# Kernel optimization log

Hardware: AMD Instinct MI355X
Metric: run time of the kernel (lower is better)

## Reference

```python
import jax, jax.numpy as jnp
import numpy as np

DIM = 3072
HEADS = 24
HD = 128  # head_dim
RANK = 64
COND = 1024      # (512//8)*(512//8)*16//64
BLOCK = 2048     # main latent tokens
SEQ = BLOCK + COND
NIP = 64         # image_emb tokens
LORA_W = 1.0     # lora_weights[0]
ALPHA_SCALE = 1.0  # network_alpha / rank = 64/64
IP_SCALE = 1.0


def setup_inputs() -> dict:
    key = jax.random.key(0)
    ks = jax.random.split(key, 21)
    d = {}
    d["hidden_states"] = jax.random.normal(ks[0], (1, SEQ, DIM), jnp.float32)
    d["image_emb"] = jax.random.normal(ks[1], (1, NIP, DIM), jnp.float32)
    d["rope_cos"] = jax.random.uniform(ks[2], (SEQ, HD), jnp.float32)
    d["rope_sin"] = jax.random.uniform(ks[3], (SEQ, HD), jnp.float32)
    d["wq"] = jax.random.normal(ks[4], (DIM, DIM), jnp.float32) * 0.02
    d["bq"] = jax.random.normal(ks[5], (DIM,), jnp.float32) * 0.02
    d["wk"] = jax.random.normal(ks[6], (DIM, DIM), jnp.float32) * 0.02
    d["bk"] = jax.random.normal(ks[7], (DIM,), jnp.float32) * 0.02
    d["wv"] = jax.random.normal(ks[8], (DIM, DIM), jnp.float32) * 0.02
    d["bv"] = jax.random.normal(ks[9], (DIM,), jnp.float32) * 0.02
    d["norm_q_w"] = jax.random.uniform(ks[10], (HD,), jnp.float32, 0.5, 1.5)
    d["norm_k_w"] = jax.random.uniform(ks[11], (HD,), jnp.float32, 0.5, 1.5)
    d["q_down"] = jax.random.normal(ks[12], (RANK, DIM), jnp.float32) / RANK
    d["q_up"] = jax.random.normal(ks[13], (DIM, RANK), jnp.float32) * 0.02
    d["k_down"] = jax.random.normal(ks[14], (RANK, DIM), jnp.float32) / RANK
    d["k_up"] = jax.random.normal(ks[15], (DIM, RANK), jnp.float32) * 0.02
    d["v_down"] = jax.random.normal(ks[16], (RANK, DIM), jnp.float32) / RANK
    d["v_up"] = jax.random.normal(ks[17], (DIM, RANK), jnp.float32) * 0.02
    d["wk_ip"] = jax.random.normal(ks[18], (DIM, DIM), jnp.float32) * 0.02
    d["wv_ip"] = jax.random.normal(ks[19], (DIM, DIM), jnp.float32) * 0.02
    return d


def _rmsnorm(x, w, eps):
    v = jnp.mean(jnp.square(x), axis=-1, keepdims=True)
    y = x * jax.lax.rsqrt(v + eps)
    return y if w is None else y * w


def _heads(x, b):  # (B,S,DIM) -> (B,H,S,HD)
    return x.reshape(b, -1, HEADS, HD).transpose(0, 2, 1, 3)


def _rope(x, cos, sin):
    # diffusers apply_rotary_emb, use_real, unbind_dim=-1
    x1 = x[..., 0::2]
    x2 = x[..., 1::2]
    rot = jnp.stack([-x2, x1], axis=-1).reshape(x.shape)
    return x * cos[None, None] + rot * sin[None, None]


def _sdpa(q, k, v, bias=None):
    s = jnp.einsum("bhqd,bhkd->bhqk", q, k) / jnp.sqrt(jnp.float32(q.shape[-1]))
    if bias is not None:
        s = s + bias
    p = jax.nn.softmax(s, axis=-1)
    return jnp.einsum("bhqk,bhkd->bhqd", p, v)


def reference(hidden_states, image_emb, rope_cos, rope_sin,
              wq, bq, wk, bk, wv, bv, norm_q_w, norm_k_w,
              q_down, q_up, k_down, k_up, v_down, v_up, wk_ip, wv_ip):
    B = hidden_states.shape[0]

    # base QKV projections
    q = hidden_states @ wq.T + bq
    k = hidden_states @ wk.T + bk
    v = hidden_states @ wv.T + bv

    # original (pre-LoRA, pre-norm, pre-RoPE) query on the main block for IP attention
    original_query = _heads(hidden_states[:, :BLOCK] @ wq.T + bq, B)

    # masked LoRA add (n_loras=1): only tokens [BLOCK, BLOCK+COND) contribute
    pos = jnp.arange(SEQ)
    tok_mask = ((pos >= BLOCK) & (pos < BLOCK + COND)).astype(hidden_states.dtype)
    hm = hidden_states * tok_mask[None, :, None]
    q = q + LORA_W * ALPHA_SCALE * ((hm @ q_down.T) @ q_up.T)
    k = k + LORA_W * ALPHA_SCALE * ((hm @ k_down.T) @ k_up.T)
    v = v + LORA_W * ALPHA_SCALE * ((hm @ v_down.T) @ v_up.T)

    q = _heads(q, B)
    k = _heads(k, B)
    v = _heads(v, B)

    # per-head RMSNorm (attn.norm_q / attn.norm_k, eps=1e-6 in Flux)
    q = _rmsnorm(q, norm_q_w, 1e-6)
    k = _rmsnorm(k, norm_k_w, 1e-6)

    # IP-adapter cross attention with the original query
    ip_k = _rmsnorm(_heads(image_emb @ wk_ip.T, B), None, 1e-5)
    ip_v = _heads(image_emb @ wv_ip.T, B)
    ip_out = _sdpa(original_query, ip_k, ip_v)  # (B,H,BLOCK,HD)
    ip_out = ip_out.transpose(0, 2, 1, 3).reshape(B, -1, DIM)

    # RoPE on q/k
    q = _rope(q, rope_cos, rope_sin)
    k = _rope(k, rope_cos, rope_sin)

    # attention bias: main-block queries see everything; cond queries only their own block
    m = jnp.ones((SEQ, SEQ), jnp.float32)
    m = m.at[:BLOCK, :].set(0.0)
    m = m.at[BLOCK:BLOCK + COND, BLOCK:BLOCK + COND].set(0.0)
    bias = (m * -1e20)[None, None]

    out = _sdpa(q, k, v, bias)  # (B,H,SEQ,HD)
    out = out.transpose(0, 2, 1, 3).reshape(B, SEQ, DIM)

    main = out[:, :BLOCK, :] + IP_SCALE * ip_out
    return main
```

## Files before the change

### kernel.cpp

```cpp
#include <hip/hip_runtime.h>
#include <stdint.h>

#define DIM 3072
#define HEADS 24
#define HD 128
#define RANKN 64
#define CONDN 1024
#define BLK 2048
#define SEQN 3072
#define NIPN 64

typedef __attribute__((ext_vector_type(8))) short s8v;
typedef __attribute__((ext_vector_type(4))) float fx4;

static __device__ __forceinline__ unsigned short f2bf(float f){
  union{float f; unsigned u;} v; v.f=f;
  unsigned r = v.u + 0x7FFFu + ((v.u>>16)&1u);
  return (unsigned short)(r>>16);
}
static __device__ __forceinline__ float bf2f(unsigned short b){
  union{unsigned u; float f;} v; v.u = ((unsigned)b) << 16;
  return v.f;
}

#define GL16(g,l) __builtin_amdgcn_global_load_lds((const __attribute__((address_space(1))) void*)(g), (__attribute__((address_space(3))) void*)(l), 16, 0, 0)
#define MFMA(a,b,c) __builtin_amdgcn_mfma_f32_16x16x32_bf16((a),(b),(c),0,0,0)

__global__ __launch_bounds__(256) void cvt_f32_bf16(const float* __restrict__ src,
                                                    unsigned short* __restrict__ dst, int n4){
  int i = blockIdx.x*256 + threadIdx.x;
  if (i < n4){
    float4 v = ((const float4*)src)[i];
    ushort4 o;
    o.x = f2bf(v.x); o.y = f2bf(v.y); o.z = f2bf(v.z); o.w = f2bf(v.w);
    ((ushort4*)dst)[i] = o;
  }
}

__global__ __launch_bounds__(256) void lora_down_g(const unsigned short* __restrict__ A,
                                                   const unsigned short* __restrict__ D0,
                                                   const unsigned short* __restrict__ D1,
                                                   unsigned short* __restrict__ outb){
  __shared__ unsigned short As[128*64];
  __shared__ unsigned short Bs[64*64];
  int tid = threadIdx.x, lane = tid & 63, w = tid >> 6;
  int l15 = lane & 15, l16 = lane >> 4;
  int z = blockIdx.z;
  int m0 = blockIdx.y * 128;
  const unsigned short* Dw = z ? D1 : D0;
  int wr = w * 32;
  fx4 acc[2][4] = {};
  for (int kt = 0; kt < DIM; kt += 64){
    #pragma unroll
    for (int i = 0; i < 4; i++){
      int p = i*256 + tid;
      int row = p >> 3, cc = p & 7;
      int gc = cc ^ (row & 7);
      GL16(A + (size_t)(m0+row)*DIM + kt + gc*8, As + p*8);
    }
    #pragma unroll
    for (int i = 0; i < 2; i++){
      int p = i*256 + tid;
      int row = p >> 3, cc = p & 7;
      int gc = cc ^ (row & 7);
      GL16(Dw + (size_t)row*DIM + kt + gc*8, Bs + p*8);
    }
    __syncthreads();
    #pragma unroll
    for (int kk = 0; kk < 2; kk++){
      s8v af[2], bfr[4];
      #pragma unroll
      for (int t = 0; t < 2; t++){
        int rowa = wr + t*16 + l15;
        int ca = (kk*4 + l16) ^ (rowa & 7);
        af[t] = *(const s8v*)(As + rowa*64 + ca*8);
      }
      #pragma unroll
      for (int t = 0; t < 4; t++){
        int rowb = t*16 + l15;
        int cb = (kk*4 + l16) ^ (rowb & 7);
        bfr[t] = *(const s8v*)(Bs + rowb*64 + cb*8);
      }
      #pragma unroll
      for (int mt = 0; mt < 2; mt++)
        #pragma unroll
        for (int nt = 0; nt < 4; nt++)
          acc[mt][nt] = MFMA(af[mt], bfr[nt], acc[mt][nt]);
    }
    __syncthreads();
  }
  #pragma unroll
  for (int mt = 0; mt < 2; mt++)
    #pragma unroll
    for (int j = 0; j < 4; j++){
      int row = m0 + wr + mt*16 + l16*4 + j;
      #pragma unroll
      for (int nt = 0; nt < 4; nt++){
        int col = nt*16 + l15;
        outb[((size_t)z*CONDN + row)*64 + col] = f2bf(acc[mt][nt][j]);
      }
    }
}

__global__ __launch_bounds__(512, 2) void gemm_256(
    const unsigned short* __restrict__ hs_bf,
    const unsigned short* __restrict__ ie_bf,
    const unsigned short* __restrict__ Wq,
    const unsigned short* __restrict__ Wk,
    const unsigned short* __restrict__ Wv,
    const unsigned short* __restrict__ Wik,
    const unsigned short* __restrict__ Wiv,
    const float* __restrict__ bq, const float* __restrict__ bk, const float* __restrict__ bv,
    const unsigned short* __restrict__ downb,
    const unsigned short* __restrict__ upk,
    const unsigned short* __restrict__ upv,
    unsigned short* __restrict__ qb, unsigned short* __restrict__ kb, unsigned short* __restrict__ vb,
    float* __restrict__ ipk_pre, float* __restrict__ ipv_pre)
{
  __shared__ unsigned short Ab[2][16384];
  __shared__ unsigned short Bb[2][16384];
  int tid = threadIdx.x, lane = tid & 63, w = tid >> 6;
  int wm = w >> 2, wn = w & 3;
  int l15 = lane & 15, l16 = lane >> 4;

  int b = blockIdx.x;
  int id = (b & 7) * 51 + (b >> 3);
  int z, mt, ntile;
  if (id < 96){ z = 0; mt = id / 12; ntile = id % 12; }
  else if (id < 240){ z = 1; int r = id - 96; mt = r / 12; ntile = r % 12; }
  else if (id < 384){ z = 2; int r = id - 240; mt = r / 12; ntile = r % 12; }
  else { z = 3; int r = id - 384; mt = r / 12; ntile = r % 12; }
  const bool is_ip = (z == 3);
  int z2 = is_ip ? mt : 0;
  int m0 = is_ip ? 0 : mt * 256;
  int n0 = ntile * 256;
  const unsigned short* A = is_ip ? ie_bf : hs_bf;
  const unsigned short* B = is_ip ? (z2 ? Wiv : Wik)
                                  : (z == 0 ? Wq : (z == 1 ? Wk : Wv));

  fx4 acc[8][4] = {};
  s8v af[8], bfr[8];

  auto stA = [&](int buf, int half, int kt){
    #pragma unroll
    for (int i = 0; i < 2; i++){
      int p = i*512 + tid;
      int row = p >> 3, cc = p & 7, gc = cc ^ (row & 7);
      int ar = m0 + half*128 + row;
      if (is_ip && ar > 63) ar = 63;
      GL16(A + (size_t)ar*DIM + kt + gc*8, &Ab[buf][half*8192 + p*8]);
    }
  };
  auto stB = [&](int buf, int half, int kt){
    #pragma unroll
    for (int i = 0; i < 2; i++){
      int p = i*512 + tid;
      int row = p >> 3, cc = p & 7, gc = cc ^ (row & 7);
      GL16(B + (size_t)(n0 + half*128 + row)*DIM + kt + gc*8, &Bb[buf][half*8192 + p*8]);
    }
  };
  auto rdA = [&](int buf, int m, int kk)->s8v{
    int rl = m*16 + l15;
    return *(const s8v*)(&Ab[buf][wm*8192 + rl*64 + ((kk*4 + l16) ^ (rl & 7))*8]);
  };
  auto rdB = [&](int buf, int n, int kk)->s8v{
    int rB = wn*64 + n*16 + l15;
    return *(const s8v*)(&Bb[buf][(rB >> 7)*8192 + (rB & 127)*64 + ((kk*4 + l16) ^ (rB & 7))*8]);
  };

  stA(0,0,0); stA(0,1,0); stB(0,0,0); stB(0,1,0);

  const int NT = DIM / 64;
  for (int t = 0; t < NT; t++){
    int cur = t & 1, nxt = cur ^ 1;
    bool pf = (t + 1 < NT);
    if (pf){
      int kt1 = (t + 1) * 64;
      stA(nxt, 0, kt1); stA(nxt, 1, kt1);
      stB(nxt, 0, kt1); stB(nxt, 1, kt1);
      asm volatile("s_waitcnt vmcnt(8)" ::: "memory");
    } else {
      asm volatile("s_waitcnt vmcnt(0)" ::: "memory");
    }
    __builtin_amdgcn_s_barrier();

    #pragma unroll
    for (int m = 0; m < 4; m++){ af[m*2] = rdA(cur,m,0); af[m*2+1] = rdA(cur,m,1); }
    #pragma unroll
    for (int n = 0; n < 2; n++){ bfr[n*2] = rdB(cur,n,0); bfr[n*2+1] = rdB(cur,n,1); }
    __builtin_amdgcn_s_setprio(1);
    #pragma unroll
    for (int m = 0; m < 4; m++)
      #pragma unroll
      for (int n = 0; n < 2; n++){
        acc[m][n] = MFMA(af[m*2],   bfr[n*2],   acc[m][n]);
        acc[m][n] = MFMA(af[m*2+1], bfr[n*2+1], acc[m][n]);
      }
    __builtin_amdgcn_s_setprio(0);
    #pragma unroll
    for (int n = 2; n < 4; n++){ bfr[n*2] = rdB(cur,n,0); bfr[n*2+1] = rdB(cur,n,1); }
    __builtin_amdgcn_s_setprio(1);
    #pragma unroll
    for (int m = 0; m < 4; m++)
      #pragma unroll
      for (int n = 2; n < 4; n++){
        acc[m][n] = MFMA(af[m*2],   bfr[n*2],   acc[m][n]);
        acc[m][n] = MFMA(af[m*2+1], bfr[n*2+1], acc[m][n]);
      }
    __builtin_amdgcn_s_setprio(0);
    #pragma unroll
    for (int m = 4; m < 8; m++){ af[(m-4)*2] = rdA(cur,m,0); af[(m-4)*2+1] = rdA(cur,m,1); }
    __builtin_amdgcn_s_setprio(1);
    #pragma unroll
    for (int m = 4; m < 8; m++)
      #pragma unroll
      for (int n = 2; n < 4; n++){
        acc[m][n] = MFMA(af[(m-4)*2],   bfr[n*2],   acc[m][n]);
        acc[m][n] = MFMA(af[(m-4)*2+1], bfr[n*2+1], acc[m][n]);
      }
    #pragma unroll
    for (int m = 4; m < 8; m++)
      #pragma unroll
      for (int n = 0; n < 2; n++){
        acc[m][n] = MFMA(af[(m-4)*2],   bfr[n*2],   acc[m][n]);
        acc[m][n] = MFMA(af[(m-4)*2+1], bfr[n*2+1], acc[m][n]);
      }
    __builtin_amdgcn_s_setprio(0);
    __builtin_amdgcn_s_barrier();
  }

  if (is_ip){
    float* outp = z2 ? ipv_pre : ipk_pre;
    if (wm == 0){
      #pragma unroll
      for (int m = 0; m < 4; m++)
        #pragma unroll
        for (int j = 0; j < 4; j++){
          int row = m*16 + l16*4 + j;
          #pragma unroll
          for (int n = 0; n < 4; n++)
            outp[(size_t)row*DIM + n0 + wn*64 + n*16 + l15] = acc[m][n][j];
        }
    }
    return;
  }

  if (z >= 1 && m0 >= BLK){
    const unsigned short* dwn = downb + (size_t)(z-1)*CONDN*64 + (size_t)(m0 - BLK)*64;
    const unsigned short* up  = (z == 1) ? upk : upv;
    #pragma unroll
    for (int i = 0; i < 4; i++){
      int p = i*512 + tid;
      int row = p >> 3, cc = p & 7, gc = cc ^ (row & 7);
      GL16(dwn + (size_t)row*64 + gc*8, &Ab[0][p*8]);
      GL16(up + (size_t)(n0 + row)*64 + gc*8, &Bb[0][p*8]);
    }
    asm volatile("s_waitcnt vmcnt(0)" ::: "memory");
    __builtin_amdgcn_s_barrier();
    #pragma unroll
    for (int kk = 0; kk < 2; kk++){
      s8v aL[8], bL[4];
      #pragma unroll
      for (int m = 0; m < 8; m++){
        int rA = wm*128 + m*16 + l15;
        aL[m] = *(const s8v*)(&Ab[0][rA*64 + ((kk*4 + l16) ^ (rA & 7))*8]);
      }
      #pragma unroll
      for (int n = 0; n < 4; n++){
        int rB = wn*64 + n*16 + l15;
        bL[n] = *(const s8v*)(&Bb[0][rB*64 + ((kk*4 + l16) ^ (rB & 7))*8]);
      }
      #pragma unroll
      for (int m = 0; m < 8; m++)
        #pragma unroll
        for (int n = 0; n < 4; n++)
          acc[m][n] = MFMA(aL[m], bL[n], acc[m][n]);
    }
  }

  {
    const float* bias = z == 0 ? bq : (z == 1 ? bk : bv);
    unsigned short* C = z == 0 ? qb : (z == 1 ? kb : vb);
    float bv4[4];
    #pragma unroll
    for (int n = 0; n < 4; n++) bv4[n] = bias[n0 + wn*64 + n*16 + l15];
    #pragma unroll
    for (int m = 0; m < 8; m++)
      #pragma unroll
      for (int j = 0; j < 4; j++){
        int row = m0 + wm*128 + m*16 + l16*4 + j;
        unsigned short* crow = C + (size_t)row*DIM;
        #pragma unroll
        for (int n = 0; n < 4; n++)
          crow[n0 + wn*64 + n*16 + l15] = f2bf(acc[m][n][j] + bv4[n]);
      }
  }
}

__global__ __launch_bounds__(256) void norm_rope(const unsigned short* __restrict__ src,
                                                 unsigned short* __restrict__ dst,
                                                 const float* __restrict__ wt,
                                                 const float* __restrict__ rc,
                                                 const float* __restrict__ rs,
                                                 int S, float qscale){
  int tid = threadIdx.x, lane = tid & 63, w = tid >> 6;
  int r = blockIdx.x*4 + w;
  int pos = r % S, h = r / S;
  const unsigned short* x = src + (size_t)pos*DIM + h*HD;
  ushort2 xv2 = *(const ushort2*)(x + 2*lane);
  float x0 = bf2f(xv2.x), x1 = bf2f(xv2.y);
  float ss = x0*x0 + x1*x1;
  #pragma unroll
  for (int o = 1; o < 64; o <<= 1) ss += __shfl_xor(ss, o);
  float rr = rsqrtf(ss*(1.f/128.f) + 1e-6f);
  float y0 = x0*rr*wt[2*lane], y1 = x1*rr*wt[2*lane+1];
  float2 cv = *(const float2*)(rc + (size_t)pos*HD + 2*lane);
  float2 sv = *(const float2*)(rs + (size_t)pos*HD + 2*lane);
  float o0 = (y0*cv.x - y1*sv.x)*qscale;
  float o1 = (y1*cv.y + y0*sv.y)*qscale;
  ushort2 ov; ov.x = f2bf(o0); ov.y = f2bf(o1);
  *(ushort2*)(dst + ((size_t)h*S + pos)*HD + 2*lane) = ov;
}

__global__ __launch_bounds__(256) void ipk_norm_bf(const float* __restrict__ src,
                                                   unsigned short* __restrict__ dst){
  int tid = threadIdx.x, lane = tid & 63, w = tid >> 6;
  int r = blockIdx.x*4 + w;
  int pos = r / HEADS, h = r % HEADS;
  const float* x = src + (size_t)pos*DIM + h*HD;
  float2 xv = *(const float2*)(x + 2*lane);
  float ss = xv.x*xv.x + xv.y*xv.y;
  #pragma unroll
  for (int o = 1; o < 64; o <<= 1) ss += __shfl_xor(ss, o);
  float rr = rsqrtf(ss*(1.f/128.f) + 1e-5f);
  ushort2 ov; ov.x = f2bf(xv.x*rr); ov.y = f2bf(xv.y*rr);
  *(ushort2*)(dst + ((size_t)h*NIPN + pos)*HD + 2*lane) = ov;
}

__global__ __launch_bounds__(256) void ipv_transpose(const float* __restrict__ ipv,
                                                     unsigned short* __restrict__ vt){
  int h = blockIdx.x, tid = threadIdx.x;
  #pragma unroll
  for (int i = 0; i < 32; i++){
    int idx = i*256 + tid;
    int d = idx >> 6, key = idx & 63;
    vt[((size_t)h*HD + d)*64 + key] = f2bf(ipv[(size_t)key*DIM + h*HD + d]);
  }
}

__global__ __launch_bounds__(256) void v_transpose(const unsigned short* __restrict__ v,
                                                   unsigned short* __restrict__ Vt){
  __shared__ unsigned short t[64][137];
  int h = blockIdx.y, p0 = blockIdx.x*64, tid = threadIdx.x;
  int dcol = tid & 127, prow2 = tid >> 7;
  #pragma unroll
  for (int i = 0; i < 32; i++){
    int pos = i*2 + prow2;
    t[pos][dcol] = v[(size_t)(p0+pos)*DIM + h*HD + dcol];
  }
  __syncthreads();
  int pos = tid & 63, dbase = tid >> 6;
  #pragma unroll
  for (int i = 0; i < 32; i++){
    int d = i*4 + dbase;
    Vt[((size_t)h*HD + d)*SEQN + p0 + pos] = t[pos][d];
  }
}

__global__ __launch_bounds__(256) void ip_attn_m(const unsigned short* __restrict__ qb,
                                                 const unsigned short* __restrict__ ipk_bf,
                                                 const unsigned short* __restrict__ ipv_t,
                                                 float* __restrict__ out){
  __shared__ unsigned short Ks[64*HD];
  __shared__ unsigned short Vs[HD*64];
  __shared__ unsigned short Ps[4][16*64];
  int tid = threadIdx.x, lane = tid & 63, w = tid >> 6;
  int l15 = lane & 15, l16 = lane >> 4;
  int h = blockIdx.y;
  int q0 = blockIdx.x*64 + w*16;
  const unsigned short* Kh = ipk_bf + (size_t)h*NIPN*HD;
  const unsigned short* Vh = ipv_t + (size_t)h*HD*NIPN;

  #pragma unroll
  for (int i = 0; i < 4; i++){
    int p = i*256 + tid;
    int row = p >> 4, cc = p & 15;
    int gc = cc ^ (row & 7);
    GL16(Kh + (size_t)row*HD + gc*8, Ks + p*8);
  }
  #pragma unroll
  for (int i = 0; i < 4; i++){
    int p = i*256 + tid;
    int row = p >> 3, cc = p & 7;
    int gc = cc ^ (row & 7);
    GL16(Vh + (size_t)row*64 + gc*8, Vs + p*8);
  }

  s8v qf[4];
  #pragma unroll
  for (int kf = 0; kf < 4; kf++)
    qf[kf] = *(const s8v*)(qb + (size_t)(q0 + l15)*DIM + h*HD + kf*32 + l16*8);
  __syncthreads();

  fx4 s[4] = {};
  #pragma unroll
  for (int ct = 0; ct < 4; ct++){
    #pragma unroll
    for (int kk = 0; kk < 4; kk++){
      int row = ct*16 + l15;
      int c = (kk*4 + l16) ^ (row & 7);
      s8v b = *(const s8v*)(Ks + row*HD + c*8);
      s[ct] = MFMA(qf[kk], b, s[ct]);
    }
  }
  const float SC = 0.08838834764831845f;
  float lrow[4];
  #pragma unroll
  for (int j = 0; j < 4; j++){
    #pragma unroll
    for (int ct = 0; ct < 4; ct++) s[ct][j] *= SC;
    float v = fmaxf(fmaxf(s[0][j], s[1][j]), fmaxf(s[2][j], s[3][j]));
    #pragma unroll
    for (int o2 = 1; o2 < 16; o2 <<= 1) v = fmaxf(v, __shfl_xor(v, o2));
    float sum = 0.f;
    #pragma unroll
    for (int ct = 0; ct < 4; ct++){
      float p = __expf(s[ct][j] - v);
      s[ct][j] = p;
      sum += p;
    }
    #pragma unroll
    for (int o2 = 1; o2 < 16; o2 <<= 1) sum += __shfl_xor(sum, o2);
    lrow[j] = sum;
  }

  #pragma unroll
  for (int ct = 0; ct < 4; ct++)
    #pragma unroll
    for (int j = 0; j < 4; j++){
      int row = l16*4 + j;
      int cidx = ct*16 + l15;
      Ps[w][row*64 + (((cidx>>3) ^ (row&7))<<3) + (cidx&7)] = f2bf(s[ct][j]);
    }
  asm volatile("s_waitcnt lgkmcnt(0)" ::: "memory");
  s8v pa[2];
  #pragma unroll
  for (int kk = 0; kk < 2; kk++){
    int c = (kk*4 + l16) ^ (l15 & 7);
    pa[kk] = *(const s8v*)(&Ps[w][l15*64 + c*8]);
  }
  fx4 o[8] = {};
  #pragma unroll
  for (int nt = 0; nt < 8; nt++){
    #pragma unroll
    for (int kk = 0; kk < 2; kk++){
      int row = nt*16 + l15;
      int c = (kk*4 + l16) ^ (row & 7);
      s8v bv = *(const s8v*)(Vs + row*64 + c*8);
      o[nt] = MFMA(pa[kk], bv, o[nt]);
    }
  }
  #pragma unroll
  for (int nt = 0; nt < 8; nt++)
    #pragma unroll
    for (int j = 0; j < 4; j++){
      int row = q0 + l16*4 + j;
      int d = nt*16 + l15;
      out[(size_t)row*DIM + h*HD + d] = o[nt][j] / lrow[j];
    }
}

#define QB 128
#define KVB 64
#define PSTR 72
__global__ __launch_bounds__(512, 4) void flash_attn_split(const unsigned short* __restrict__ Qn,
                                                           const unsigned short* __restrict__ Kn,
                                                           const unsigned short* __restrict__ Vt,
                                                           float* __restrict__ po0,
                                                           float* __restrict__ po1,
                                                           float* __restrict__ pm,
                                                           float* __restrict__ pl){
  __shared__ unsigned short Ks[KVB*HD];
  __shared__ unsigned short Vs[HD*KVB];
  __shared__ unsigned short Ps[8][16*PSTR];
  int tid = threadIdx.x, lane = tid & 63, w = tid >> 6;
  int l15 = lane & 15, l16 = lane >> 4;
  int b = blockIdx.x;
  int swz = (b & 7) * 96 + (b >> 3);
  int sp = swz / 384;
  int rem = swz - sp*384;
  int h = rem >> 4;
  int qt = rem & 15;
  int q0 = qt*QB + w*16;
  const unsigned short* Qh = Qn + (size_t)h*BLK*HD;
  const unsigned short* Kh = Kn + (size_t)h*SEQN*HD;
  const unsigned short* Vh = Vt + (size_t)h*HD*SEQN;
  const int kvbase = sp * (SEQN/2);
  const int NT = (SEQN/2) / KVB;

  s8v qf[4];
  #pragma unroll
  for (int kf = 0; kf < 4; kf++)
    qf[kf] = *(const s8v*)(Qh + (size_t)(q0 + l15)*HD + kf*32 + l16*8);

  fx4 o[8] = {};
  float mrow[4], lrow[4];
  #pragma unroll
  for (int j = 0; j < 4; j++){ mrow[j] = -1e30f; lrow[j] = 0.f; }

  for (int t = 0; t < NT; t++){
    int kv0 = kvbase + t*KVB;
    #pragma unroll
    for (int i = 0; i < 2; i++){
      int p = i*512 + tid;
      int row = p >> 4, cc = p & 15;
      int gc = cc ^ (row & 7);
      GL16(Kh + (size_t)(kv0+row)*HD + gc*8, Ks + p*8);
    }
    #pragma unroll
    for (int i = 0; i < 2; i++){
      int p = i*512 + tid;
      int row = p >> 3, cc = p & 7;
      int gc = cc ^ (row & 7);
      GL16(Vh + (size_t)row*SEQN + kv0 + gc*8, Vs + p*8);
    }
    __syncthreads();

    fx4 s[4] = {};
    #pragma unroll
    for (int ct = 0; ct < 4; ct++){
      #pragma unroll
      for (int kk = 0; kk < 4; kk++){
        int row = ct*16 + l15;
        int c = (kk*4 + l16) ^ (row & 7);
        s8v bb = *(const s8v*)(Ks + row*HD + c*8);
        s[ct] = MFMA(qf[kk], bb, s[ct]);
      }
    }
    float pmax[4], rssum[4];
    #pragma unroll
    for (int j = 0; j < 4; j++){
      float v = fmaxf(fmaxf(s[0][j], s[1][j]), fmaxf(s[2][j], s[3][j]));
      #pragma unroll
      for (int o2 = 1; o2 < 16; o2 <<= 1) v = fmaxf(v, __shfl_xor(v, o2));
      pmax[j] = v;
      rssum[j] = 0.f;
    }
    float need = 0.f;
    #pragma unroll
    for (int j = 0; j < 4; j++) need = fmaxf(need, pmax[j] - mrow[j]);
    if (__any(need > 8.f)){
      float alpha[4];
      #pragma unroll
      for (int j = 0; j < 4; j++){
        float mnew = fmaxf(mrow[j], pmax[j]);
        alpha[j] = __expf(mrow[j] - mnew);
        mrow[j] = mnew;
      }
      #pragma unroll
      for (int nt = 0; nt < 8; nt++)
        #pragma unroll
        for (int j = 0; j < 4; j++) o[nt][j] *= alpha[j];
      #pragma unroll
      for (int j = 0; j < 4; j++) lrow[j] *= alpha[j];
    }
    #pragma unroll
    for (int ct = 0; ct < 4; ct++)
      #pragma unroll
      for (int j = 0; j < 4; j++){
        float p = __expf(s[ct][j] - mrow[j]);
        s[ct][j] = p;
        rssum[j] += p;
      }
    #pragma unroll
    for (int j = 0; j < 4; j++){
      #pragma unroll
      for (int o2 = 1; o2 < 16; o2 <<= 1) rssum[j] += __shfl_xor(rssum[j], o2);
      lrow[j] += rssum[j];
    }

    #pragma unroll
    for (int ct = 0; ct < 4; ct++)
      #pragma unroll
      for (int j = 0; j < 4; j++){
        int row = l16*4 + j;
        int cidx = ct*16 + l15;
        Ps[w][row*PSTR + cidx] = f2bf(s[ct][j]);
      }
    asm volatile("s_waitcnt lgkmcnt(0)" ::: "memory");
    s8v pa[2];
    #pragma unroll
    for (int kk = 0; kk < 2; kk++)
      pa[kk] = *(const s8v*)(&Ps[w][l15*PSTR + (kk*4 + l16)*8]);
    #pragma unroll
    for (int nt = 0; nt < 8; nt++){
      #pragma unroll
      for (int kk = 0; kk < 2; kk++){
        int row = nt*16 + l15;
        int c = (kk*4 + l16) ^ (row & 7);
        s8v bvv = *(const s8v*)(Vs + row*KVB + c*8);
        o[nt] = MFMA(pa[kk], bvv, o[nt]);
      }
    }
    __syncthreads();
  }

  float* pop = sp ? po1 : po0;
  #pragma unroll
  for (int nt = 0; nt < 8; nt++)
    #pragma unroll
    for (int j = 0; j < 4; j++){
      int row = q0 + l16*4 + j;
      int d = nt*16 + l15;
      pop[((size_t)h*BLK + row)*HD + d] = o[nt][j];
    }
  if (l15 == 0){
    #pragma unroll
    for (int j = 0; j < 4; j++){
      int row = q0 + l16*4 + j;
      pm[(size_t)sp*HEADS*BLK + h*BLK + row] = mrow[j];
      pl[(size_t)sp*HEADS*BLK + h*BLK + row] = lrow[j];
    }
  }
}

__global__ __launch_bounds__(256) void flash_merge(const float* __restrict__ po0,
                                                   const float* __restrict__ po1,
                                                   const float* __restrict__ pm,
                                                   const float* __restrict__ pl,
                                                   float* __restrict__ out){
  int tid = threadIdx.x, lane = tid & 63, w = tid >> 6;
  int r = blockIdx.x*4 + w;
  int h = r >> 11, pos = r & 2047;
  float m0 = pm[r], m1 = pm[HEADS*BLK + r];
  float l0 = pl[r], l1 = pl[HEADS*BLK + r];
  float mx = fmaxf(m0, m1);
  float a0 = __expf(m0 - mx), a1 = __expf(m1 - mx);
  float li = 1.f / (l0*a0 + l1*a1);
  float s0 = a0*li, s1 = a1*li;
  size_t base = ((size_t)h*BLK + pos)*HD + 2*lane;
  float2 x0 = *(const float2*)(po0 + base);
  float2 x1 = *(const float2*)(po1 + base);
  float* op = out + (size_t)pos*DIM + h*HD + 2*lane;
  float2 cv = *(const float2*)op;
  cv.x += x0.x*s0 + x1.x*s1;
  cv.y += x0.y*s0 + x1.y*s1;
  *(float2*)op = cv;
}

extern "C" void kernel_launch(void* const* d_in, const int* in_sizes, int n_in,
                              void* d_out, int out_size, void* d_ws, size_t ws_size,
                              hipStream_t stream){
  (void)in_sizes; (void)n_in; (void)out_size;
  const float* hs       = (const float*)d_in[0];
  const float* image_emb= (const float*)d_in[1];
  const float* rope_cos = (const float*)d_in[2];
  const float* rope_sin = (const float*)d_in[3];
  const float* wq = (const float*)d_in[4];
  const float* bq = (const float*)d_in[5];
  const float* wk = (const float*)d_in[6];
  const float* bk = (const float*)d_in[7];
  const float* wv = (const float*)d_in[8];
  const float* bv = (const float*)d_in[9];
  const float* norm_q_w = (const float*)d_in[10];
  const float* norm_k_w = (const float*)d_in[11];
  const float* k_down = (const float*)d_in[14];
  const float* k_up   = (const float*)d_in[15];
  const float* v_down = (const float*)d_in[16];
  const float* v_up   = (const float*)d_in[17];
  const float* wk_ip  = (const float*)d_in[18];
  const float* wv_ip  = (const float*)d_in[19];
  float* out = (float*)d_out;

  char* ws = (char*)d_ws;
  size_t off = 0;
  auto alloc = [&](size_t bytes){ void* p = ws + off; off += (bytes + 255) & ~(size_t)255; return p; };
  unsigned short* hs_bf = (unsigned short*)alloc((size_t)SEQN*DIM*2);
  unsigned short* ie_bf = (unsigned short*)alloc((size_t)NIPN*DIM*2);
  unsigned short* w_bf[5];
  for (int i = 0; i < 5; i++) w_bf[i] = (unsigned short*)alloc((size_t)DIM*DIM*2);
  unsigned short* lw_bf[4];
  for (int i = 0; i < 4; i++) lw_bf[i] = (unsigned short*)alloc((size_t)RANKN*DIM*2);
  unsigned short* downb = (unsigned short*)alloc((size_t)2*CONDN*RANKN*2);
  unsigned short* qb = (unsigned short*)alloc((size_t)BLK*DIM*2);
  unsigned short* kb = (unsigned short*)alloc((size_t)SEQN*DIM*2);
  unsigned short* vb = (unsigned short*)alloc((size_t)SEQN*DIM*2);
  float* ipk_pre = (float*)alloc((size_t)NIPN*DIM*4);
  float* ipv_pre = (float*)alloc((size_t)NIPN*DIM*4);
  unsigned short* ipk_bf = (unsigned short*)alloc((size_t)HEADS*NIPN*HD*2);
  unsigned short* ipv_t  = (unsigned short*)alloc((size_t)HEADS*HD*NIPN*2);
  float* po0 = (float*)alloc((size_t)HEADS*BLK*HD*4);
  float* po1 = (float*)alloc((size_t)HEADS*BLK*HD*4);
  float* pm  = (float*)alloc((size_t)2*HEADS*BLK*4);
  float* pl  = (float*)alloc((size_t)2*HEADS*BLK*4);
  if (off > ws_size) return;

  unsigned short* Qn = w_bf[0];
  unsigned short* Kn = w_bf[1];
  unsigned short* Vt = w_bf[2];

  int n4;
  n4 = SEQN*DIM/4;
  cvt_f32_bf16<<<(n4+255)/256, 256, 0, stream>>>(hs, hs_bf, n4);
  n4 = NIPN*DIM/4;
  cvt_f32_bf16<<<(n4+255)/256, 256, 0, stream>>>(image_emb, ie_bf, n4);

  n4 = DIM*DIM/4;
  cvt_f32_bf16<<<(n4+255)/256, 256, 0, stream>>>(wq, w_bf[0], n4);
  cvt_f32_bf16<<<(n4+255)/256, 256, 0, stream>>>(wk, w_bf[1], n4);
  cvt_f32_bf16<<<(n4+255)/256, 256, 0, stream>>>(wv, w_bf[2], n4);
  cvt_f32_bf16<<<(n4+255)/256, 256, 0, stream>>>(wk_ip, w_bf[3], n4);
  cvt_f32_bf16<<<(n4+255)/256, 256, 0, stream>>>(wv_ip, w_bf[4], n4);

  n4 = RANKN*DIM/4;
  cvt_f32_bf16<<<(n4+255)/256, 256, 0, stream>>>(k_down, lw_bf[0], n4);
  cvt_f32_bf16<<<(n4+255)/256, 256, 0, stream>>>(v_down, lw_bf[1], n4);
  cvt_f32_bf16<<<(n4+255)/256, 256, 0, stream>>>(k_up,   lw_bf[2], n4);
  cvt_f32_bf16<<<(n4+255)/256, 256, 0, stream>>>(v_up,   lw_bf[3], n4);

  lora_down_g<<<dim3(1, CONDN/128, 2), 256, 0, stream>>>(hs_bf + (size_t)BLK*DIM,
      lw_bf[0], lw_bf[1], downb);

  gemm_256<<<408, 512, 0, stream>>>(hs_bf, ie_bf,
      w_bf[0], w_bf[1], w_bf[2], w_bf[3], w_bf[4],
      bq, bk, bv, downb, lw_bf[2], lw_bf[3],
      qb, kb, vb, ipk_pre, ipv_pre);

  ipk_norm_bf<<<(NIPN*HEADS)/4, 256, 0, stream>>>(ipk_pre, ipk_bf);
  ipv_transpose<<<HEADS, 256, 0, stream>>>(ipv_pre, ipv_t);

  const float SC = 0.08838834764831845f;
  norm_rope<<<(BLK*HEADS)/4, 256, 0, stream>>>(qb, Qn, norm_q_w, rope_cos, rope_sin, BLK, SC);
  norm_rope<<<(SEQN*HEADS)/4, 256, 0, stream>>>(kb, Kn, norm_k_w, rope_cos, rope_sin, SEQN, 1.0f);
  v_transpose<<<dim3(SEQN/64, HEADS), 256, 0, stream>>>(vb, Vt);

  ip_attn_m<<<dim3(BLK/64, HEADS), 256, 0, stream>>>(qb, ipk_bf, ipv_t, out);
  flash_attn_split<<<768, 512, 0, stream>>>(Qn, Kn, Vt, po0, po1, pm, pl);
  flash_merge<<<(HEADS*BLK)/4, 256, 0, stream>>>(po0, po1, pm, pl, out);
}
```

Before: 547.8 us.

## Halve K-tile in QKV GEMM to shrink LDS and raise occupancy

The 256x256 GEMM's K step drops from 64 to 32. Shared memory falls from 128KB to 64KB in a single buffer with a 4-column XOR swizzle, and launch bounds ask for 4 waves per SIMD instead of 2. The inner loop now loads 12 fragments and issues 32 MFMAs per step, with no staged interleaving of LDS reads and MFMAs. The aim is more resident blocks to hide latency. The cost is twice as many barriers and K iterations, and more register pressure, since the 128-float accumulator must fit under the tighter launch bound and may spill.

```diff
diff --git a/kernel.cpp b/kernel.cpp
--- a/kernel.cpp
+++ b/kernel.cpp
@@ -102,7 +102,7 @@
     }
 }
 
-__global__ __launch_bounds__(512, 2) void gemm_256(
+__global__ __launch_bounds__(512, 4) void gemm_256(
     const unsigned short* __restrict__ hs_bf,
     const unsigned short* __restrict__ ie_bf,
     const unsigned short* __restrict__ Wq,
@@ -117,8 +117,7 @@
     unsigned short* __restrict__ qb, unsigned short* __restrict__ kb, unsigned short* __restrict__ vb,
     float* __restrict__ ipk_pre, float* __restrict__ ipv_pre)
 {
-  __shared__ unsigned short Ab[2][16384];
-  __shared__ unsigned short Bb[2][16384];
+  __shared__ unsigned short S[32768];
   int tid = threadIdx.x, lane = tid & 63, w = tid >> 6;
   int wm = w >> 2, wn = w & 3;
   int l15 = lane & 15, l16 = lane >> 4;
@@ -139,92 +138,60 @@
                                   : (z == 0 ? Wq : (z == 1 ? Wk : Wv));
 
   fx4 acc[8][4] = {};
-  s8v af[8], bfr[8];
-
-  auto stA = [&](int buf, int half, int kt){
+  s8v af[8], bfr[4];
+
+  auto stA = [&](int buf, int kt){
     #pragma unroll
     for (int i = 0; i < 2; i++){
       int p = i*512 + tid;
-      int row = p >> 3, cc = p & 7, gc = cc ^ (row & 7);
-      int ar = m0 + half*128 + row;
+      int row = p >> 2, cc = p & 3, gc = cc ^ (row & 3);
+      int ar = m0 + row;
       if (is_ip && ar > 63) ar = 63;
-      GL16(A + (size_t)ar*DIM + kt + gc*8, &Ab[buf][half*8192 + p*8]);
+      GL16(A + (size_t)ar*DIM + kt + gc*8, S + buf*8192 + p*8);
     }
   };
-  auto stB = [&](int buf, int half, int kt){
+  auto stB = [&](int buf, int kt){
     #pragma unroll
     for (int i = 0; i < 2; i++){
       int p = i*512 + tid;
-      int row = p >> 3, cc = p & 7, gc = cc ^ (row & 7);
-      GL16(B + (size_t)(n0 + half*128 + row)*DIM + kt + gc*8, &Bb[buf][half*8192 + p*8]);
+      int row = p >> 2, cc = p & 3, gc = cc ^ (row & 3);
+      GL16(B + (size_t)(n0 + row)*DIM + kt + gc*8, S + 16384 + buf*8192 + p*8);
     }
   };
-  auto rdA = [&](int buf, int m, int kk)->s8v{
-    int rl = m*16 + l15;
-    return *(const s8v*)(&Ab[buf][wm*8192 + rl*64 + ((kk*4 + l16) ^ (rl & 7))*8]);
+  auto rdA = [&](int buf, int m)->s8v{
+    int rl = wm*128 + m*16 + l15;
+    return *(const s8v*)(S + buf*8192 + rl*32 + ((l16 ^ (rl & 3))*8));
   };
-  auto rdB = [&](int buf, int n, int kk)->s8v{
+  auto rdB = [&](int buf, int n)->s8v{
     int rB = wn*64 + n*16 + l15;
-    return *(const s8v*)(&Bb[buf][(rB >> 7)*8192 + (rB & 127)*64 + ((kk*4 + l16) ^ (rB & 7))*8]);
+    return *(const s8v*)(S + 16384 + buf*8192 + rB*32 + ((l16 ^ (rB & 3))*8));
   };
 
-  stA(0,0,0); stA(0,1,0); stB(0,0,0); stB(0,1,0);
-
-  const int NT = DIM / 64;
+  stA(0, 0); stB(0, 0);
+
+  const int NT = DIM / 32;
   for (int t = 0; t < NT; t++){
     int cur = t & 1, nxt = cur ^ 1;
     bool pf = (t + 1 < NT);
     if (pf){
-      int kt1 = (t + 1) * 64;
-      stA(nxt, 0, kt1); stA(nxt, 1, kt1);
-      stB(nxt, 0, kt1); stB(nxt, 1, kt1);
-      asm volatile("s_waitcnt vmcnt(8)" ::: "memory");
+      int kt1 = (t + 1) * 32;
+      stA(nxt, kt1); stB(nxt, kt1);
+      asm volatile("s_waitcnt vmcnt(4)" ::: "memory");
     } else {
       asm volatile("s_waitcnt vmcnt(0)" ::: "memory");
     }
     __builtin_amdgcn_s_barrier();
 
     #pragma unroll
-    for (int m = 0; m < 4; m++){ af[m*2] = rdA(cur,m,0); af[m*2+1] = rdA(cur,m,1); }
-    #pragma unroll
-    for (int n = 0; n < 2; n++){ bfr[n*2] = rdB(cur,n,0); bfr[n*2+1] = rdB(cur,n,1); }
+    for (int n = 0; n < 4; n++) bfr[n] = rdB(cur, n);
+    #pragma unroll
+    for (int m = 0; m < 8; m++) af[m] = rdA(cur, m);
     __builtin_amdgcn_s_setprio(1);
     #pragma unroll
-    for (int m = 0; m < 4; m++)
-      #pragma unroll
-      for (int n = 0; n < 2; n++){
-        acc[m][n] = MFMA(af[m*2],   bfr[n*2],   acc[m][n]);
-        acc[m][n] = MFMA(af[m*2+1], bfr[n*2+1], acc[m][n]);
-      }
-    __builtin_amdgcn_s_setprio(0);
-    #pragma unroll
-    for (int n = 2; n < 4; n++){ bfr[n*2] = rdB(cur,n,0); bfr[n*2+1] = rdB(cur,n,1); }
-    __builtin_amdgcn_s_setprio(1);
-    #pragma unroll
-    for (int m = 0; m < 4; m++)
-      #pragma unroll
-      for (int n = 2; n < 4; n++){
-        acc[m][n] = MFMA(af[m*2],   bfr[n*2],   acc[m][n]);
-        acc[m][n] = MFMA(af[m*2+1], bfr[n*2+1], acc[m][n]);
-      }
-    __builtin_amdgcn_s_setprio(0);
-    #pragma unroll
-    for (int m = 4; m < 8; m++){ af[(m-4)*2] = rdA(cur,m,0); af[(m-4)*2+1] = rdA(cur,m,1); }
-    __builtin_amdgcn_s_setprio(1);
-    #pragma unroll
-    for (int m = 4; m < 8; m++)
-      #pragma unroll
-      for (int n = 2; n < 4; n++){
-        acc[m][n] = MFMA(af[(m-4)*2],   bfr[n*2],   acc[m][n]);
-        acc[m][n] = MFMA(af[(m-4)*2+1], bfr[n*2+1], acc[m][n]);
-      }
-    #pragma unroll
-    for (int m = 4; m < 8; m++)
-      #pragma unroll
-      for (int n = 0; n < 2; n++){
-        acc[m][n] = MFMA(af[(m-4)*2],   bfr[n*2],   acc[m][n]);
-        acc[m][n] = MFMA(af[(m-4)*2+1], bfr[n*2+1], acc[m][n]);
-      }
+    for (int m = 0; m < 8; m++)
+      #pragma unroll
+      for (int n = 0; n < 4; n++)
+        acc[m][n] = MFMA(af[m], bfr[n], acc[m][n]);
     __builtin_amdgcn_s_setprio(0);
     __builtin_amdgcn_s_barrier();
   }
@@ -252,8 +219,8 @@
     for (int i = 0; i < 4; i++){
       int p = i*512 + tid;
       int row = p >> 3, cc = p & 7, gc = cc ^ (row & 7);
-      GL16(dwn + (size_t)row*64 + gc*8, &Ab[0][p*8]);
-      GL16(up + (size_t)(n0 + row)*64 + gc*8, &Bb[0][p*8]);
+      GL16(dwn + (size_t)row*64 + gc*8, S + p*8);
+      GL16(up + (size_t)(n0 + row)*64 + gc*8, S + 16384 + p*8);
     }
     asm volatile("s_waitcnt vmcnt(0)" ::: "memory");
     __builtin_amdgcn_s_barrier();
@@ -263,12 +230,12 @@
       #pragma unroll
       for (int m = 0; m < 8; m++){
         int rA = wm*128 + m*16 + l15;
-        aL[m] = *(const s8v*)(&Ab[0][rA*64 + ((kk*4 + l16) ^ (rA & 7))*8]);
+        aL[m] = *(const s8v*)(S + rA*64 + ((kk*4 + l16) ^ (rA & 7))*8);
       }
       #pragma unroll
       for (int n = 0; n < 4; n++){
         int rB = wn*64 + n*16 + l15;
-        bL[n] = *(const s8v*)(&Bb[0][rB*64 + ((kk*4 + l16) ^ (rB & 7))*8]);
+        bL[n] = *(const s8v*)(S + 16384 + rB*64 + ((kk*4 + l16) ^ (rB & 7))*8);
       }
       #pragma unroll
       for (int m = 0; m < 8; m++)
```

Result: slower. 1.978 ms (+261.1%).
